# Performance work log

Hardware: AMD Instinct MI355X
Metric: run time of the kernel (lower is better)

Reference implementation:

```python
import jax, jax.numpy as jnp
import numpy as np

EPS = 1e-5
K = 20
LRELU = 0.2


def _bn(x, g, b, ch_axis):
    # inference BatchNorm with running_mean=0, running_var=1
    shape = [1] * x.ndim
    shape[ch_axis] = -1
    scale = (g / jnp.sqrt(1.0 + EPS)).reshape(shape)
    bias = b.reshape(shape)
    return x * scale + bias


def _lrelu(x):
    return jnp.where(x > 0, x, LRELU * x)


def _edge_conv(x, W, g, b):
    # x: (B, C, N) -> (B, C_out, N)
    B, C, N = x.shape
    xt = jnp.swapaxes(x, 1, 2)                      # (B, N, C)
    inner = -2.0 * jnp.einsum('bnc,bmc->bnm', xt, xt)
    xx = jnp.sum(xt * xt, axis=2)                   # (B, N)
    pdist = -xx[:, :, None] - inner - xx[:, None, :]  # negative sq dist (B,N,N)
    idx = jax.lax.top_k(pdist, K)[1]                # (B, N, K) nearest (incl. self)
    # gather neighbor features per batch: (C, N) indexed by (N, K) -> (C, N, K)
    neighbors = jax.vmap(lambda xf, id_: xf[:, id_])(x, idx)  # (B, C, N, K)
    center = jnp.broadcast_to(x[..., None], (B, C, N, K))
    edge = jnp.concatenate([center, neighbors - center], axis=1)  # (B, 2C, N, K)
    h = jnp.einsum('oc,bcnk->bonk', W, edge)        # 1x1 conv, no bias
    h = _lrelu(_bn(h, g, b, 1))
    return jnp.max(h, axis=-1)                      # (B, C_out, N)


def setup_inputs() -> dict:
    key = jax.random.key(0)
    ks = jax.random.split(key, 24)
    B, N = 4, 2048
    d = {}
    d['points'] = jax.random.normal(ks[0], (B, N, 3), dtype=jnp.float32)

    def w(k_, shape):
        return 0.1 * jax.random.normal(k_, shape, dtype=jnp.float32)

    def gam(k_, c):
        return 1.0 + 0.1 * jax.random.normal(k_, (c,), dtype=jnp.float32)

    def bet(k_, c):
        return 0.05 * jax.random.normal(k_, (c,), dtype=jnp.float32)

    # EdgeConv blocks: (out, 2*in)
    d['w1'], d['g1'], d['b1'] = w(ks[1], (64, 6)), gam(ks[2], 64), bet(ks[3], 64)
    d['w2'], d['g2'], d['b2'] = w(ks[4], (64, 128)), gam(ks[5], 64), bet(ks[6], 64)
    d['w3'], d['g3'], d['b3'] = w(ks[7], (128, 128)), gam(ks[8], 128), bet(ks[9], 128)
    d['w4'], d['g4'], d['b4'] = w(ks[10], (256, 256)), gam(ks[11], 256), bet(ks[12], 256)
    # conv5 1x1: 512 -> 1024
    d['w5'], d['g5'], d['b5'] = w(ks[13], (1024, 512)), gam(ks[14], 1024), bet(ks[15], 1024)
    # fc: 2048 -> 512 -> 256
    d['fw1'], d['fb1'] = w(ks[16], (512, 2048)), 0.05 * jax.random.normal(ks[17], (512,), dtype=jnp.float32)
    d['g6'], d['b6'] = gam(ks[18], 512), bet(ks[19], 512)
    d['fw2'], d['fb2'] = w(ks[20], (256, 512)), 0.05 * jax.random.normal(ks[21], (256,), dtype=jnp.float32)
    d['g7'], d['b7'] = gam(ks[22], 256), bet(ks[23], 256)
    return d


def reference(points, w1, g1, b1, w2, g2, b2, w3, g3, b3, w4, g4, b4,
              w5, g5, b5, fw1, fb1, g6, b6, fw2, fb2, g7, b7):
    x = jnp.swapaxes(points[:, :, :3], 1, 2)        # (B, 3, N)
    x1 = _edge_conv(x, w1, g1, b1)                  # (B, 64, N)
    x2 = _edge_conv(x1, w2, g2, b2)                 # (B, 64, N)
    x3 = _edge_conv(x2, w3, g3, b3)                 # (B, 128, N)
    x4 = _edge_conv(x3, w4, g4, b4)                 # (B, 256, N)
    h = jnp.concatenate([x1, x2, x3, x4], axis=1)   # (B, 512, N)
    h = _lrelu(_bn(jnp.einsum('oc,bcn->bon', w5, h), g5, b5, 1))  # (B, 1024, N)
    h_max = jnp.max(h, axis=-1)
    h_avg = jnp.mean(h, axis=-1)
    f = jnp.concatenate([h_max, h_avg], axis=1)     # (B, 2048)
    f = _lrelu(_bn(f @ fw1.T + fb1, g6, b6, 1))     # dropout = identity (eval)
    f = _bn(f @ fw2.T + fb2, g7, b7, 1)
    return f                                        # (B, 256)
```

## Files before the change

### kernel.cpp

```cpp
#include <hip/hip_runtime.h>
#include <hip/hip_bf16.h>
#include <float.h>

#define N_PTS 2048
#define B_SZ  4
#define KNN   20
#define LRELU_S 0.2f
#define FT    512
#define NPOOL 8

typedef __hip_bfloat16 bf16;
typedef __attribute__((ext_vector_type(8))) short short8v;
typedef __attribute__((ext_vector_type(4))) short short4v;
typedef __attribute__((ext_vector_type(4))) float floatx4;

__device__ __forceinline__ float b2f(const bf16 v) { return __bfloat162float(v); }
__device__ __forceinline__ float ldf(const float* p) { return *p; }
__device__ __forceinline__ float ldf(const bf16* p)  { return __bfloat162float(*p); }
__device__ __forceinline__ short8v ld8(const bf16* p) { return *(const short8v*)p; }
__device__ __forceinline__ unsigned umin(unsigned a, unsigned b) { return a < b ? a : b; }
__device__ __forceinline__ short bfbits(float f) {
    bf16 t = __float2bfloat16(f);
    return *reinterpret_cast<short*>(&t);
}

__device__ __forceinline__ void gload16(const void* g, void* l) {
    __builtin_amdgcn_global_load_lds(
        (const __attribute__((address_space(1))) void*)g,
        (__attribute__((address_space(3))) void*)l, 16, 0, 0);
}

__device__ __forceinline__ int sniff_body(const unsigned short* pts_hw) {
    int sane = 0;
    for (int j = 0; j < 64; ++j) {
        unsigned short v = pts_hw[2 * j];
        int e = (v >> 7) & 0xFF;
        if (e >= 100 && e <= 140) ++sane;
    }
    return (sane >= 32) ? 1 : 0;
}

__global__ void k_sniff(const unsigned short* __restrict__ pts_hw, int* __restrict__ flag) {
    if (threadIdx.x != 0 || blockIdx.x != 0) return;
    *flag = sniff_body(pts_hw);
}

struct WPack {
    const void* src[23];
    int off[24];
    int rows[23];
    int cols[23];
};

__device__ __forceinline__ void repack_body(const WPack& wp, int isb,
                                            float* __restrict__ dst, int i, int limit) {
    if (i >= limit) return;
    int lo = 0, hi = 23;
    while (lo + 1 < hi) { int mid = (lo + hi) >> 1; if (i >= wp.off[mid]) lo = mid; else hi = mid; }
    int j = i - wp.off[lo];
    float v = isb ? b2f(((const bf16*)wp.src[lo])[j]) : ((const float*)wp.src[lo])[j];
    int dj = j;
    int cols = wp.cols[lo];
    if (cols) dj = (j % cols) * wp.rows[lo] + (j / cols);
    dst[wp.off[lo] + dj] = v;
}

template<int C, int COUT>
__device__ __forceinline__ void wsplit_body(const void* __restrict__ W, int isb,
                                            bf16* __restrict__ dst, int i) {
    if (i >= COUT * C) return;
    int o = i / C, c = i % C;
    float w1 = isb ? b2f(((const bf16*)W)[(size_t)o * 2 * C + c])
                   : ((const float*)W)[(size_t)o * 2 * C + c];
    float w2 = isb ? b2f(((const bf16*)W)[(size_t)o * 2 * C + C + c])
                   : ((const float*)W)[(size_t)o * 2 * C + C + c];
    float wd = w1 - w2;
    bf16 h2 = __float2bfloat16(w2);
    bf16 hd = __float2bfloat16(wd);
    dst[i]                = h2;
    dst[COUT * C + i]     = __float2bfloat16(w2 - b2f(h2));
    dst[2 * COUT * C + i] = hd;
    dst[3 * COUT * C + i] = __float2bfloat16(wd - b2f(hd));
}

__device__ __forceinline__ void w5split_body(const void* __restrict__ W, int isb,
                                             bf16* __restrict__ dst, int i) {
    if (i >= 1024 * 512) return;
    float w = isb ? b2f(((const bf16*)W)[i]) : ((const float*)W)[i];
    bf16 h = __float2bfloat16(w);
    dst[i] = h;
    dst[1024 * 512 + i] = __float2bfloat16(w - b2f(h));
}

__device__ __forceinline__ void transpose_body(const void* __restrict__ pts, int isb,
                                               float* __restrict__ x0, int i) {
    if (i >= B_SZ * N_PTS) return;
    int b = i / N_PTS, n = i % N_PTS;
    for (int c = 0; c < 3; ++c) {
        size_t s = ((size_t)b * N_PTS + n) * 3 + c;
        float v = isb ? b2f(((const bf16*)pts)[s]) : ((const float*)pts)[s];
        x0[((size_t)b * 3 + c) * N_PTS + n] = v;
    }
}

__global__ void k_prep(WPack wp, float* __restrict__ wf, int rlimit,
                       const void* __restrict__ w2s, bf16* __restrict__ wsp2,
                       const void* __restrict__ w3s, bf16* __restrict__ wsp3,
                       const void* __restrict__ w4s, bf16* __restrict__ wsp4,
                       const void* __restrict__ w5s, bf16* __restrict__ w5sp,
                       const void* __restrict__ pts, float* __restrict__ x0,
                       int* __restrict__ flagout) {
    __shared__ int sfl;
    if (threadIdx.x == 0) {
        int f = sniff_body((const unsigned short*)pts);
        sfl = f;
        if (blockIdx.x == 0) *flagout = f;
    }
    __syncthreads();
    const int isb = sfl;
    const int nbrep = (rlimit + 255) >> 8;
    int ib = blockIdx.x, t = threadIdx.x;
    if (ib < nbrep) { repack_body(wp, isb, wf, ib * 256 + t, rlimit); return; }
    ib -= nbrep;
    if (ib < 16)   { wsplit_body<64, 64>(w2s, isb, wsp2, ib * 256 + t); return; }
    ib -= 16;
    if (ib < 32)   { wsplit_body<64, 128>(w3s, isb, wsp3, ib * 256 + t); return; }
    ib -= 32;
    if (ib < 128)  { wsplit_body<128, 256>(w4s, isb, wsp4, ib * 256 + t); return; }
    ib -= 128;
    if (ib < 2048) { w5split_body(w5s, isb, w5sp, ib * 256 + t); return; }
    ib -= 2048;
    transpose_body(pts, isb, x0, ib * 256 + t);
}

__global__ void k_repack(WPack wp, const int* __restrict__ flag, float* __restrict__ dst, int limit) {
    repack_body(wp, *flag, dst, blockIdx.x * blockDim.x + threadIdx.x, limit);
}
__global__ void k_transpose(const void* __restrict__ pts, const int* __restrict__ flag,
                            float* __restrict__ x0) {
    transpose_body(pts, *flag, x0, blockIdx.x * blockDim.x + threadIdx.x);
}

__device__ __forceinline__ void load32(const float* row, int mbase, float* r) {
    const float4* p = (const float4*)(row + mbase);
#pragma unroll
    for (int i = 0; i < 8; ++i) {
        float4 f = p[i];
        r[4 * i + 0] = f.x; r[4 * i + 1] = f.y; r[4 * i + 2] = f.z; r[4 * i + 3] = f.w;
    }
}
__device__ __forceinline__ void load32(const bf16* row, int mbase, float* r) {
    const uint4* p = (const uint4*)(row + mbase);
#pragma unroll
    for (int i = 0; i < 4; ++i) {
        uint4 u = p[i];
        r[8 * i + 0] = __uint_as_float(u.x << 16);
        r[8 * i + 1] = __uint_as_float(u.x & 0xFFFF0000u);
        r[8 * i + 2] = __uint_as_float(u.y << 16);
        r[8 * i + 3] = __uint_as_float(u.y & 0xFFFF0000u);
        r[8 * i + 4] = __uint_as_float(u.z << 16);
        r[8 * i + 5] = __uint_as_float(u.z & 0xFFFF0000u);
        r[8 * i + 6] = __uint_as_float(u.w << 16);
        r[8 * i + 7] = __uint_as_float(u.w & 0xFFFF0000u);
    }
}

__device__ __forceinline__ void s2ins(unsigned k, unsigned& m1, unsigned& m2) {
    unsigned lo = umin(m1, k);
    unsigned hi = (m1 < k) ? k : m1;
    m1 = lo;
    m2 = umin(m2, hi);
}

__device__ __forceinline__ void select20x2(const unsigned* ka, const unsigned* kb,
                                           int* outA, int* outB, int lane) {
    const unsigned SENT = 0xFFFFFFFFu;
    unsigned a1 = SENT, a2 = SENT, b1 = SENT, b2 = SENT;
#pragma unroll
    for (int j = 0; j < 32; ++j) {
        s2ins(ka[j], a1, a2);
        s2ins(kb[j], b1, b2);
    }
#pragma unroll 1
    for (int k = 0; k < KNN; ++k) {
        unsigned va = a1, vb = b1;
#pragma unroll
        for (int off = 32; off >= 1; off >>= 1) {
            va = umin(va, (unsigned)__shfl_xor((int)va, off));
            vb = umin(vb, (unsigned)__shfl_xor((int)vb, off));
        }
        if (lane == 0) { outA[k] = (int)(va & 2047u); outB[k] = (int)(vb & 2047u); }
        if (a1 == va) { a1 = a2; a2 = SENT; }
        if (b1 == vb) { b1 = b2; b2 = SENT; }
        if (a1 == SENT) {
#pragma unroll
            for (int j = 0; j < 32; ++j) {
                unsigned t = (ka[j] > va) ? ka[j] : SENT;
                s2ins(t, a1, a2);
            }
        }
        if (b1 == SENT) {
#pragma unroll
            for (int j = 0; j < 32; ++j) {
                unsigned t = (kb[j] > vb) ? kb[j] : SENT;
                s2ins(t, b1, b2);
            }
        }
    }
}

__global__ __launch_bounds__(256) void k_knn3(const float* __restrict__ x0,
                                              int* __restrict__ idx) {
    __shared__ float qf[8][3];
    int ib = blockIdx.x;
    int b  = ib / (N_PTS / 8);
    int q0 = (ib % (N_PTS / 8)) * 8;
    const float* xb = x0 + (size_t)b * 3 * N_PTS;

    if (threadIdx.x < 24) {
        int q = threadIdx.x / 3, c = threadIdx.x % 3;
        qf[q][c] = xb[(size_t)c * N_PTS + q0 + q];
    }
    __syncthreads();

    int w = threadIdx.x >> 6, lane = threadIdx.x & 63;
    int qa = q0 + 2 * w;
    int mbase = lane * 32;

    float da[32], db[32];
#pragma unroll
    for (int j = 0; j < 32; ++j) { da[j] = 0.f; db[j] = 0.f; }
#pragma unroll
    for (int c = 0; c < 3; ++c) {
        float r[32];
        load32(xb + (size_t)c * N_PTS, mbase, r);
        float qac = qf[2 * w][c], qbc = qf[2 * w + 1][c];
#pragma unroll
        for (int j = 0; j < 32; ++j) {
            float ta = r[j] - qac; da[j] = fmaf(ta, ta, da[j]);
            float tb = r[j] - qbc; db[j] = fmaf(tb, tb, db[j]);
        }
    }
    unsigned ka[32], kb[32];
#pragma unroll
    for (int j = 0; j < 32; ++j) {
        ka[j] = (__float_as_uint(da[j]) & 0xFFFFF800u) | (unsigned)(mbase + j);
        kb[j] = (__float_as_uint(db[j]) & 0xFFFFF800u) | (unsigned)(mbase + j);
    }
    select20x2(ka, kb, idx + ((size_t)b * N_PTS + qa) * KNN,
               idx + ((size_t)b * N_PTS + qa + 1) * KNN, lane);
}

template<typename T, int C>
__global__ __launch_bounds__(256) void k_knn(const T* __restrict__ x, int bstride,
                                             int* __restrict__ idx) {
    __shared__ float qf[4][C];
    int ib = blockIdx.x;
    int b  = ib / (N_PTS / 4);
    int q0 = (ib % (N_PTS / 4)) * 4;
    const T* xb = x + (size_t)b * bstride;

    for (int t = threadIdx.x; t < 4 * C; t += 256) {
        int pt = t / C, c = t % C;
        qf[pt][c] = ldf(&xb[(size_t)c * N_PTS + (q0 + pt)]);
    }
    __syncthreads();

    int w = threadIdx.x >> 6, lane = threadIdx.x & 63;
    int q = q0 + w;
    int mbase = lane * 32;

    float v[32];
#pragma unroll
    for (int j = 0; j < 32; ++j) v[j] = 0.f;

    for (int c = 0; c < C; ++c) {
        float qc = qf[w][c];
        float r[32];
        load32(xb + (size_t)c * N_PTS, mbase, r);
#pragma unroll
        for (int j = 0; j < 32; ++j) { float t = r[j] - qc; v[j] = fmaf(t, t, v[j]); }
    }

    for (int k = 0; k < KNN; ++k) {
        float bv = FLT_MAX; int bi = 0x7FFFFFFF;
#pragma unroll
        for (int j = 0; j < 32; ++j)
            if (v[j] < bv) { bv = v[j]; bi = mbase + j; }
#pragma unroll
        for (int off = 32; off >= 1; off >>= 1) {
            float ov = __shfl_xor(bv, off);
            int   oi = __shfl_xor(bi, off);
            if (ov < bv || (ov == bv && oi < bi)) { bv = ov; bi = oi; }
        }
        if (lane == 0) idx[((size_t)b * N_PTS + q) * KNN + k] = bi;
        int wl = bi >> 5, wj = bi & 31;
        if (lane == wl) {
#pragma unroll
            for (int j = 0; j < 32; ++j) if (j == wj) v[j] = FLT_MAX;
        }
    }
}

template<int C>
__device__ __forceinline__ void gram_body(const bf16* __restrict__ featT, int c0,
                                          float* __restrict__ G,
                                          short* At, short* Bt, int ib) {
    const int KC = 64;
    int b  = ib >> 8;
    int t  = ib & 255;
    int n0 = (t >> 4) << 7;
    int m0 = (t & 15) << 7;

    int tid = threadIdx.x;
    int w = tid >> 6, lane = tid & 63;
    int rw = (w & 1) * 64, cw = (w >> 1) * 64;
    int lrow = lane & 15, quad = lane >> 4;

    floatx4 acc[4][4];
#pragma unroll
    for (int ri = 0; ri < 4; ++ri)
#pragma unroll
        for (int ci = 0; ci < 4; ++ci) acc[ri][ci] = (floatx4){0.f, 0.f, 0.f, 0.f};

    for (int ck = 0; ck < C; ck += KC) {
        __syncthreads();
#pragma unroll
        for (int it = 0; it < 4; ++it) {
            int s = tid + it * 256;
            int row = s >> 3, seg = s & 7;
            int gseg = seg ^ (row & 7);
            gload16(featT + ((size_t)(b * N_PTS + n0 + row) * FT) + c0 + ck + gseg * 8,
                    &At[(s & ~63) * 8]);
            gload16(featT + ((size_t)(b * N_PTS + m0 + row) * FT) + c0 + ck + gseg * 8,
                    &Bt[(s & ~63) * 8]);
        }
        __syncthreads();
#pragma unroll
        for (int kk = 0; kk < KC; kk += 32) {
            int ks = kk >> 3;
            short8v a[4], bb[4];
#pragma unroll
            for (int ri = 0; ri < 4; ++ri) {
                int row = rw + ri * 16 + lrow;
                int seg = (ks + quad) ^ (row & 7);
                a[ri] = *(const short8v*)&At[row * 64 + seg * 8];
            }
#pragma unroll
            for (int ci = 0; ci < 4; ++ci) {
                int row = cw + ci * 16 + lrow;
                int seg = (ks + quad) ^ (row & 7);
                bb[ci] = *(const short8v*)&Bt[row * 64 + seg * 8];
            }
#pragma unroll
            for (int ri = 0; ri < 4; ++ri)
#pragma unroll
                for (int ci = 0; ci < 4; ++ci)
                    acc[ri][ci] = __builtin_amdgcn_mfma_f32_16x16x32_bf16(a[ri], bb[ci], acc[ri][ci], 0, 0, 0);
        }
    }

#pragma unroll
    for (int ri = 0; ri < 4; ++ri)
#pragma unroll
        for (int ci = 0; ci < 4; ++ci) {
            int n = n0 + rw + ri * 16 + quad * 4;
            int m = m0 + cw + ci * 16 + lrow;
            float* gp = G + ((size_t)b * N_PTS + n) * N_PTS + m;
#pragma unroll
            for (int reg = 0; reg < 4; ++reg)
                gp[(size_t)reg * N_PTS] = acc[ri][ci][reg];
        }
}

template<int COUT, int C>
__device__ __forceinline__ void xform_body(const bf16* __restrict__ featT, int c0,
                                           const bf16* __restrict__ Wsp,
                                           bf16* __restrict__ Yh, int isb,
                                           short* Bt, int ib2) {
    const int M2 = 2 * COUT;
    const int KC = 64;
    int nt = ib2 & 63;
    int mt = ib2 >> 6;
    int tid = threadIdx.x;
    int w = tid >> 6, lane = tid & 63;
    int rw = (w & 1) * 64, cw = (w >> 1) * 64;
    int l15 = lane & 15, quad = lane >> 4;

    floatx4 acc[4][4];
#pragma unroll
    for (int ri = 0; ri < 4; ++ri)
#pragma unroll
        for (int ci = 0; ci < 4; ++ci) acc[ri][ci] = (floatx4){0.f, 0.f, 0.f, 0.f};

    for (int ck = 0; ck < C; ck += KC) {
        __syncthreads();
#pragma unroll
        for (int it = 0; it < 4; ++it) {
            int s = tid + it * 256;
            int row = s >> 3, seg = s & 7;
            int gseg = seg ^ (row & 7);
            gload16(featT + (size_t)(nt * 128 + row) * FT + c0 + ck + gseg * 8,
                    &Bt[(s & ~63) * 8]);
        }
        __syncthreads();
#pragma unroll
        for (int kk = 0; kk < KC; kk += 32) {
            int ks = kk >> 3;
            short8v bfr[4];
#pragma unroll
            for (int ci = 0; ci < 4; ++ci) {
                int row = cw + ci * 16 + l15;
                int seg = (ks + quad) ^ (row & 7);
                bfr[ci] = *(const short8v*)&Bt[row * 64 + seg * 8];
            }
#pragma unroll
            for (int ri = 0; ri < 4; ++ri) {
                int rbase = mt * 128 + rw + ri * 16;
                bool uselo = (!isb) || (rbase >= COUT);
                int mrow = rbase + l15;
                int base = (mrow < COUT) ? mrow : (mrow + COUT);
                const bf16* hi = Wsp + (size_t)base * C + ck + kk + quad * 8;
                short8v ah = ld8(hi);
                short8v al;
                if (uselo) al = ld8(hi + (size_t)COUT * C);
#pragma unroll
                for (int ci = 0; ci < 4; ++ci) {
                    acc[ri][ci] = __builtin_amdgcn_mfma_f32_16x16x32_bf16(ah, bfr[ci], acc[ri][ci], 0, 0, 0);
                    if (uselo)
                        acc[ri][ci] = __builtin_amdgcn_mfma_f32_16x16x32_bf16(al, bfr[ci], acc[ri][ci], 0, 0, 0);
                }
            }
        }
    }

#pragma unroll
    for (int ri = 0; ri < 4; ++ri)
#pragma unroll
        for (int ci = 0; ci < 4; ++ci) {
            int n = nt * 128 + cw + ci * 16 + l15;
            int m = mt * 128 + rw + ri * 16 + quad * 4;
            short4v o4;
            o4[0] = bfbits(acc[ri][ci][0]);
            o4[1] = bfbits(acc[ri][ci][1]);
            o4[2] = bfbits(acc[ri][ci][2]);
            o4[3] = bfbits(acc[ri][ci][3]);
            *(short4v*)(Yh + (size_t)n * M2 + m) = o4;
        }
}

template<int C, int COUT>
__global__ __launch_bounds__(256) void k_gx(const bf16* __restrict__ featT, int c0,
        const bf16* __restrict__ Wsp, float* __restrict__ G, bf16* __restrict__ Yh,
        const int* __restrict__ flag) {
    __shared__ __align__(16) short lds[2 * 128 * 64];
    int ib = blockIdx.x;
    if (ib < B_SZ * 256) {
        gram_body<C>(featT, c0, G, lds, lds + 128 * 64, ib);
    } else {
        xform_body<COUT, C>(featT, c0, Wsp, Yh, *flag, lds, ib - B_SZ * 256);
    }
}

template<int COUT>
__global__ __launch_bounds__(256) void k_selgmax(const float* __restrict__ G,
        const float* __restrict__ xxin, const bf16* __restrict__ Yh,
        const float* __restrict__ gam, const float* __restrict__ bet,
        bf16* __restrict__ featT, int c0f, float* __restrict__ xxout) {
    const int M2 = 2 * COUT;
    const int OT = COUT / 64;
    __shared__ int sidx[8][KNN];

    int ib = blockIdx.x;
    int b  = ib / (N_PTS / 8);
    int q0 = (ib % (N_PTS / 8)) * 8;
    int w = threadIdx.x >> 6, lane = threadIdx.x & 63;
    int qa = q0 + 2 * w;
    const float* gA = G + ((size_t)b * N_PTS + qa) * N_PTS;
    const float* gB = gA + N_PTS;
    const float* xr = xxin + (size_t)b * N_PTS;
    float xqa = xr[qa], xqb = xr[qa + 1];

    unsigned ka[32], kb[32];
#pragma unroll
    for (int r = 0; r < 8; ++r) {
        int m0 = r * 256 + (lane << 2);
        float4 x4 = *(const float4*)(xr + m0);
        float4 a4 = *(const float4*)(gA + m0);
        float4 b4 = *(const float4*)(gB + m0);
        float s;
        s = fmaf(-2.f, a4.x, x4.x) + xqa; s = fmaxf(s, 0.f);
        ka[4 * r + 0] = (__float_as_uint(s) & 0xFFFFF800u) | (unsigned)(m0 + 0);
        s = fmaf(-2.f, a4.y, x4.y) + xqa; s = fmaxf(s, 0.f);
        ka[4 * r + 1] = (__float_as_uint(s) & 0xFFFFF800u) | (unsigned)(m0 + 1);
        s = fmaf(-2.f, a4.z, x4.z) + xqa; s = fmaxf(s, 0.f);
        ka[4 * r + 2] = (__float_as_uint(s) & 0xFFFFF800u) | (unsigned)(m0 + 2);
        s = fmaf(-2.f, a4.w, x4.w) + xqa; s = fmaxf(s, 0.f);
        ka[4 * r + 3] = (__float_as_uint(s) & 0xFFFFF800u) | (unsigned)(m0 + 3);
        s = fmaf(-2.f, b4.x, x4.x) + xqb; s = fmaxf(s, 0.f);
        kb[4 * r + 0] = (__float_as_uint(s) & 0xFFFFF800u) | (unsigned)(m0 + 0);
        s = fmaf(-2.f, b4.y, x4.y) + xqb; s = fmaxf(s, 0.f);
        kb[4 * r + 1] = (__float_as_uint(s) & 0xFFFFF800u) | (unsigned)(m0 + 1);
        s = fmaf(-2.f, b4.z, x4.z) + xqb; s = fmaxf(s, 0.f);
        kb[4 * r + 2] = (__float_as_uint(s) & 0xFFFFF800u) | (unsigned)(m0 + 2);
        s = fmaf(-2.f, b4.w, x4.w) + xqb; s = fmaxf(s, 0.f);
        kb[4 * r + 3] = (__float_as_uint(s) & 0xFFFFF800u) | (unsigned)(m0 + 3);
    }
    select20x2(ka, kb, &sidx[2 * w][0], &sidx[2 * w + 1][0], lane);
    __syncthreads();

    size_t iA = (size_t)b * N_PTS + qa;
    const float inv = rsqrtf(1.0f + 1e-5f);
    float yda[OT], ydb[OT], scl[OT], bis[OT], mxa[OT], mxb[OT];
#pragma unroll
    for (int j = 0; j < OT; ++j) {
        int o = lane + 64 * j;
        yda[j] = b2f(Yh[iA * M2 + COUT + o]);
        ydb[j] = b2f(Yh[(iA + 1) * M2 + COUT + o]);
        scl[j] = gam[o] * inv;
        bis[j] = bet[o];
        mxa[j] = -FLT_MAX; mxb[j] = -FLT_MAX;
    }
    const bf16* Yb = Yh + (size_t)b * N_PTS * M2;
#pragma unroll
    for (int k = 0; k < KNN; ++k) {
        int m0 = sidx[2 * w][k] & (N_PTS - 1);
        int m1 = sidx[2 * w + 1][k] & (N_PTS - 1);
        const bf16* r0 = Yb + (size_t)m0 * M2;
        const bf16* r1 = Yb + (size_t)m1 * M2;
#pragma unroll
        for (int j = 0; j < OT; ++j) {
            int o = lane + 64 * j;
            float ha = (yda[j] + b2f(r0[o])) * scl[j] + bis[j];
            ha = ha > 0.f ? ha : LRELU_S * ha;
            mxa[j] = fmaxf(mxa[j], ha);
            float hb = (ydb[j] + b2f(r1[o])) * scl[j] + bis[j];
            hb = hb > 0.f ? hb : LRELU_S * hb;
            mxb[j] = fmaxf(mxb[j], hb);
        }
    }
    float sa = 0.f, sb = 0.f;
#pragma unroll
    for (int j = 0; j < OT; ++j) {
        bf16 va = __float2bfloat16(mxa[j]);
        bf16 vb = __float2bfloat16(mxb[j]);
        featT[iA * FT + c0f + lane + 64 * j] = va;
        featT[(iA + 1) * FT + c0f + lane + 64 * j] = vb;
        if (xxout) {
            float pa = b2f(va); sa = fmaf(pa, pa, sa);
            float pb = b2f(vb); sb = fmaf(pb, pb, sb);
        }
    }
    if (xxout) {
#pragma unroll
        for (int off = 32; off >= 1; off >>= 1) {
            sa += __shfl_xor(sa, off);
            sb += __shfl_xor(sb, off);
        }
        if (lane == 0) { xxout[iA] = sa; xxout[iA + 1] = sb; }
    }
}

template<typename T, int C, int COUT, bool WF>
__global__ __launch_bounds__(256) void k_edgeconv(const T* __restrict__ x, int bstride,
                           const int* __restrict__ idx,
                           const float* __restrict__ Wt,
                           const float* __restrict__ gam,
                           const float* __restrict__ bet,
                           bf16* __restrict__ out, int ostride,
                           bf16* __restrict__ featT, int c0f,
                           float* __restrict__ xxout) {
    const int PT = 4;
    const int OT = COUT / 64;
    const int CP = (C + 3) & ~3;
    __shared__ float sh[PT][KNN + 1][CP];

    int ib = blockIdx.x;
    int b  = ib / (N_PTS / PT);
    int n0 = (ib % (N_PTS / PT)) * PT;
    const T* xb = x + (size_t)b * bstride;

    const int TOT = PT * (KNN + 1) * C;
    for (int t = threadIdx.x; t < TOT; t += 256) {
        int pt = t / ((KNN + 1) * C);
        int r  = t % ((KNN + 1) * C);
        int row = r / C, c = r % C;
        int n = n0 + pt;
        int m = (row == 0) ? n
                           : (idx[((size_t)b * N_PTS + n) * KNN + (row - 1)] & (N_PTS - 1));
        sh[pt][row][c] = ldf(&xb[(size_t)c * N_PTS + m]);
    }
    __syncthreads();

    int w = threadIdx.x >> 6, lane = threadIdx.x & 63;
    int n = n0 + w;

    constexpr int KT = (OT >= 4) ? 10 : 20;
    constexpr int NPASS = KNN / KT;

    float base[OT];
    float mx[OT];
#pragma unroll
    for (int j = 0; j < OT; ++j) { base[j] = 0.f; mx[j] = -FLT_MAX; }

    const float inv = rsqrtf(1.0f + 1e-5f);

#pragma unroll
    for (int pass = 0; pass < NPASS; ++pass) {
        float acc[OT][KT];
#pragma unroll
        for (int j = 0; j < OT; ++j)
#pragma unroll
            for (int k = 0; k < KT; ++k) acc[j][k] = 0.f;

        for (int c = 0; c < C; ++c) {
            float xq = sh[w][0][c];
            float w2v[OT];
#pragma unroll
            for (int j = 0; j < OT; ++j)
                w2v[j] = Wt[(size_t)(C + c) * COUT + lane + 64 * j];
            if (pass == 0) {
#pragma unroll
                for (int j = 0; j < OT; ++j) {
                    float w1v = Wt[(size_t)c * COUT + lane + 64 * j];
                    base[j] = fmaf(w1v - w2v[j], xq, base[j]);
                }
            }
#pragma unroll
            for (int k = 0; k < KT; ++k) {
                float nv = sh[w][1 + pass * KT + k][c];
#pragma unroll
                for (int j = 0; j < OT; ++j) acc[j][k] = fmaf(w2v[j], nv, acc[j][k]);
            }
        }

#pragma unroll
        for (int j = 0; j < OT; ++j) {
            int o = lane + 64 * j;
            float scale = gam[o] * inv, bias = bet[o];
#pragma unroll
            for (int k = 0; k < KT; ++k) {
                float h = (base[j] + acc[j][k]) * scale + bias;
                h = h > 0.f ? h : LRELU_S * h;
                mx[j] = fmaxf(mx[j], h);
            }
        }
    }

    float s = 0.f;
#pragma unroll
    for (int j = 0; j < OT; ++j) {
        int o = lane + 64 * j;
        bf16 bv = __float2bfloat16(mx[j]);
        if (!WF) out[(size_t)b * ostride + (size_t)o * N_PTS + n] = bv;
        if (WF) {
            featT[((size_t)b * N_PTS + n) * FT + c0f + o] = bv;
            float q = b2f(bv);
            s = fmaf(q, q, s);
        }
    }
    if (WF && xxout) {
#pragma unroll
        for (int off = 32; off >= 1; off >>= 1) s += __shfl_xor(s, off);
        if (lane == 0) xxout[(size_t)b * N_PTS + n] = s;
    }
}

__global__ __launch_bounds__(256) void k_conv5mfma(
        const bf16* __restrict__ featT, const bf16* __restrict__ w5sp,
        const float* __restrict__ g5, const float* __restrict__ b5,
        float* __restrict__ fmxp, float* __restrict__ fsmp,
        const int* __restrict__ flag) {
    __shared__ __align__(16) short Bt[256 * 64];
    __shared__ __align__(16) short Ah[64 * 64];
    __shared__ __align__(16) short Al[64 * 64];
    __shared__ float rmx[4][64];
    __shared__ float rsm[4][64];

    const int isb = *flag;
    int ib = blockIdx.x;
    int b  = ib / 128;
    int rem = ib % 128;
    int o0 = (rem >> 3) * 64;
    int nt = rem & 7;
    int tid = threadIdx.x;
    int w = tid >> 6, lane = tid & 63;
    int l15 = lane & 15, quad = lane >> 4;

    const bf16* Whi = w5sp;
    const bf16* Wlo = w5sp + 1024 * 512;
    const bf16* fb  = featT + (size_t)b * N_PTS * FT;
    const int nbase0 = nt * 256;

    floatx4 acc[4][4];
#pragma unroll
    for (int mi = 0; mi < 4; ++mi)
#pragma unroll
        for (int ni = 0; ni < 4; ++ni) acc[mi][ni] = (floatx4){0.f, 0.f, 0.f, 0.f};

    for (int ck = 0; ck < 512; ck += 64) {
        __syncthreads();
#pragma unroll
        for (int it = 0; it < 8; ++it) {
            int s = tid + it * 256;
            int row = s >> 3, seg = s & 7;
            int gseg = seg ^ (row & 7);
            gload16(fb + (size_t)(nbase0 + row) * FT + ck + gseg * 8,
                    &Bt[(s & ~63) * 8]);
        }
#pragma unroll
        for (int it = 0; it < 2; ++it) {
            int s = tid + it * 256;
            int row = s >> 3, seg = s & 7;
            int gseg = seg ^ (row & 7);
            gload16(Whi + (size_t)(o0 + row) * 512 + ck + gseg * 8, &Ah[(s & ~63) * 8]);
            if (!isb)
                gload16(Wlo + (size_t)(o0 + row) * 512 + ck + gseg * 8, &Al[(s & ~63) * 8]);
        }
        __syncthreads();
#pragma unroll
        for (int kk = 0; kk < 64; kk += 32) {
            int ks = kk >> 3;
            short8v bfr[4], ah[4], al[4];
#pragma unroll
            for (int ni = 0; ni < 4; ++ni) {
                int row = w * 64 + ni * 16 + l15;
                int seg = (ks + quad) ^ (row & 7);
                bfr[ni] = *(const short8v*)&Bt[row * 64 + seg * 8];
            }
#pragma unroll
            for (int mi = 0; mi < 4; ++mi) {
                int row = mi * 16 + l15;
                int seg = (ks + quad) ^ (row & 7);
                ah[mi] = *(const short8v*)&Ah[row * 64 + seg * 8];
                if (!isb) al[mi] = *(const short8v*)&Al[row * 64 + seg * 8];
            }
#pragma unroll
            for (int mi = 0; mi < 4; ++mi)
#pragma unroll
                for (int ni = 0; ni < 4; ++ni) {
                    acc[mi][ni] = __builtin_amdgcn_mfma_f32_16x16x32_bf16(ah[mi], bfr[ni], acc[mi][ni], 0, 0, 0);
                    if (!isb)
                        acc[mi][ni] = __builtin_amdgcn_mfma_f32_16x16x32_bf16(al[mi], bfr[ni], acc[mi][ni], 0, 0, 0);
                }
        }
    }

    const float inv = rsqrtf(1.0f + 1e-5f);
#pragma unroll
    for (int mi = 0; mi < 4; ++mi) {
#pragma unroll
        for (int r = 0; r < 4; ++r) {
            int o = o0 + mi * 16 + quad * 4 + r;
            float scale = g5[o] * inv, bias = b5[o];
            float mx = -FLT_MAX, sm = 0.f;
#pragma unroll
            for (int ni = 0; ni < 4; ++ni) {
                float h = acc[mi][ni][r] * scale + bias;
                h = h > 0.f ? h : LRELU_S * h;
                mx = fmaxf(mx, h);
                sm += h;
            }
#pragma unroll
            for (int off = 1; off <= 8; off <<= 1) {
                mx = fmaxf(mx, __shfl_xor(mx, off));
                sm += __shfl_xor(sm, off);
            }
            if (l15 == 0) {
                rmx[w][mi * 16 + quad * 4 + r] = mx;
                rsm[w][mi * 16 + quad * 4 + r] = sm;
            }
        }
    }
    __syncthreads();
    if (tid < 64) {
        float mx = -FLT_MAX, sm = 0.f;
#pragma unroll
        for (int ww = 0; ww < 4; ++ww) { mx = fmaxf(mx, rmx[ww][tid]); sm += rsm[ww][tid]; }
        fmxp[((size_t)b * 1024 + o0 + tid) * NPOOL + nt] = mx;
        fsmp[((size_t)b * 1024 + o0 + tid) * NPOOL + nt] = sm;
    }
}

__global__ void k_pool(const float* __restrict__ fmxp, const float* __restrict__ fsmp,
                       float* __restrict__ fvec) {
    int i = blockIdx.x * blockDim.x + threadIdx.x;
    if (i >= B_SZ * 1024) return;
    int b = i >> 10, o = i & 1023;
    float mx = -FLT_MAX, sm = 0.f;
    for (int ch = 0; ch < NPOOL; ++ch) {
        mx = fmaxf(mx, fmxp[(size_t)i * NPOOL + ch]);
        sm += fsmp[(size_t)i * NPOOL + ch];
    }
    fvec[(size_t)b * 2048 + o] = mx;
    fvec[(size_t)b * 2048 + 1024 + o] = sm * (1.0f / N_PTS);
}

__global__ __launch_bounds__(256) void k_fc1(const float* __restrict__ fvec,
        const void* __restrict__ fw1, const void* __restrict__ fb1,
        const void* __restrict__ g6,  const void* __restrict__ b6,
        const int* __restrict__ flag, float* __restrict__ tbuf) {
    __shared__ float red[4];
    int ib = blockIdx.x;
    int b = ib >> 9, o = ib & 511;
    const float* fv = fvec + (size_t)b * 2048;
    int tid = threadIdx.x;
    const int isb = *flag;
    float s = 0.f;
    if (isb) {
        const bf16* wr = (const bf16*)fw1 + (size_t)o * 2048;
        for (int j = tid; j < 2048; j += 256) s = fmaf(b2f(wr[j]), fv[j], s);
    } else {
        const float* wr = (const float*)fw1 + (size_t)o * 2048;
        for (int j = tid; j < 2048; j += 256) s = fmaf(wr[j], fv[j], s);
    }
#pragma unroll
    for (int off = 32; off >= 1; off >>= 1) s += __shfl_xor(s, off);
    if ((tid & 63) == 0) red[tid >> 6] = s;
    __syncthreads();
    if (tid == 0) {
        float fb = isb ? b2f(((const bf16*)fb1)[o]) : ((const float*)fb1)[o];
        float gg = isb ? b2f(((const bf16*)g6)[o])  : ((const float*)g6)[o];
        float bb = isb ? b2f(((const bf16*)b6)[o])  : ((const float*)b6)[o];
        float acc = fb + red[0] + red[1] + red[2] + red[3];
        float h = acc * gg * rsqrtf(1.0f + 1e-5f) + bb;
        tbuf[(size_t)b * 512 + o] = h > 0.f ? h : LRELU_S * h;
    }
}

__global__ __launch_bounds__(256) void k_fc2(const float* __restrict__ tbuf,
        const void* __restrict__ fw2, const void* __restrict__ fb2,
        const void* __restrict__ g7,  const void* __restrict__ b7,
        const int* __restrict__ flag, void* __restrict__ out) {
    __shared__ float red[4];
    int ib = blockIdx.x;
    int b = ib >> 8, o = ib & 255;
    const float* tv = tbuf + (size_t)b * 512;
    int tid = threadIdx.x;
    const int isb = *flag;
    float s;
    if (isb) {
        const bf16* wr = (const bf16*)fw2 + (size_t)o * 512;
        s = fmaf(b2f(wr[tid]), tv[tid], b2f(wr[tid + 256]) * tv[tid + 256]);
    } else {
        const float* wr = (const float*)fw2 + (size_t)o * 512;
        s = fmaf(wr[tid], tv[tid], wr[tid + 256] * tv[tid + 256]);
    }
#pragma unroll
    for (int off = 32; off >= 1; off >>= 1) s += __shfl_xor(s, off);
    if ((tid & 63) == 0) red[tid >> 6] = s;
    __syncthreads();
    if (tid == 0) {
        float fb = isb ? b2f(((const bf16*)fb2)[o]) : ((const float*)fb2)[o];
        float gg = isb ? b2f(((const bf16*)g7)[o])  : ((const float*)g7)[o];
        float bb = isb ? b2f(((const bf16*)b7)[o])  : ((const float*)b7)[o];
        float acc = fb + red[0] + red[1] + red[2] + red[3];
        float h = acc * gg * rsqrtf(1.0f + 1e-5f) + bb;
        if (isb) ((bf16*)out)[(size_t)b * 256 + o] = __float2bfloat16(h);
        else     ((float*)out)[(size_t)b * 256 + o] = h;
    }
}

#define NCH 2
__global__ __launch_bounds__(256) void k_conv5pool(const bf16* __restrict__ feat,
                            const float* __restrict__ w5,
                            const float* __restrict__ g5,
                            const float* __restrict__ b5,
                            float* __restrict__ fmxp, float* __restrict__ fsmp) {
    const int OT = 8;
    const int NT = 4;
    const int CHN = N_PTS / NCH;
    __shared__ float wl[OT][512];
    __shared__ float rmx[4][OT];
    __shared__ float rsm[4][OT];

    int ib = blockIdx.x;
    int ch = ib % NCH;
    int ot = (ib / NCH) % (1024 / OT);
    int b  = ib / (NCH * (1024 / OT));
    int o0 = ot * OT;
    const bf16* fb = feat + (size_t)b * 512 * N_PTS;

    for (int t = threadIdx.x; t < OT * 512; t += 256) {
        int o = t >> 9, c = t & 511;
        wl[o][c] = w5[(size_t)(o0 + o) * 512 + c];
    }
    __syncthreads();

    const int n0 = ch * CHN + threadIdx.x * NT;

    float acc[OT][NT];
#pragma unroll
    for (int o = 0; o < OT; ++o)
#pragma unroll
        for (int t = 0; t < NT; ++t) acc[o][t] = 0.f;

    for (int c = 0; c < 512; c += 4) {
        float fv[4][NT];
#pragma unroll
        for (int j = 0; j < 4; ++j) {
            uint2 u = *(const uint2*)(fb + (size_t)(c + j) * N_PTS + n0);
            fv[j][0] = __uint_as_float(u.x << 16);
            fv[j][1] = __uint_as_float(u.x & 0xFFFF0000u);
            fv[j][2] = __uint_as_float(u.y << 16);
            fv[j][3] = __uint_as_float(u.y & 0xFFFF0000u);
        }
#pragma unroll
        for (int o = 0; o < OT; ++o) {
            float4 wv = *(const float4*)&wl[o][c];
#pragma unroll
            for (int t = 0; t < NT; ++t) {
                acc[o][t] = fmaf(wv.x, fv[0][t], acc[o][t]);
                acc[o][t] = fmaf(wv.y, fv[1][t], acc[o][t]);
                acc[o][t] = fmaf(wv.z, fv[2][t], acc[o][t]);
                acc[o][t] = fmaf(wv.w, fv[3][t], acc[o][t]);
            }
        }
    }

    const float inv = rsqrtf(1.0f + 1e-5f);
    int w = threadIdx.x >> 6, lane = threadIdx.x & 63;
#pragma unroll
    for (int o = 0; o < OT; ++o) {
        float scale = g5[o0 + o] * inv, bias = b5[o0 + o];
        float mx = -FLT_MAX, sm = 0.f;
#pragma unroll
        for (int t = 0; t < NT; ++t) {
            float h = acc[o][t] * scale + bias;
            h = h > 0.f ? h : LRELU_S * h;
            mx = fmaxf(mx, h);
            sm += h;
        }
#pragma unroll
        for (int off = 32; off >= 1; off >>= 1) {
            mx = fmaxf(mx, __shfl_xor(mx, off));
            sm += __shfl_xor(sm, off);
        }
        if (lane == 0) { rmx[w][o] = mx; rsm[w][o] = sm; }
    }
    __syncthreads();
    if (threadIdx.x < OT) {
        int o = threadIdx.x;
        float mx = -FLT_MAX, sm = 0.f;
#pragma unroll
        for (int ww = 0; ww < 4; ++ww) { mx = fmaxf(mx, rmx[ww][o]); sm += rsm[ww][o]; }
        fmxp[((size_t)b * 1024 + o0 + o) * NCH + ch] = mx;
        fsmp[((size_t)b * 1024 + o0 + o) * NCH + ch] = sm;
    }
}

__global__ void k_head(const float* __restrict__ fmxp, const float* __restrict__ fsmp,
                       const float* __restrict__ fw1, const float* __restrict__ fb1,
                       const float* __restrict__ g6,  const float* __restrict__ b6,
                       const float* __restrict__ fw2, const float* __restrict__ fb2,
                       const float* __restrict__ g7,  const float* __restrict__ b7,
                       const int* __restrict__ flag, void* __restrict__ out) {
    __shared__ float f[2048];
    __shared__ float t[512];
    int b = blockIdx.x;
    for (int i = threadIdx.x; i < 1024; i += 256) {
        float mx = -FLT_MAX, sm = 0.f;
        for (int ch = 0; ch < NCH; ++ch) {
            mx = fmaxf(mx, fmxp[((size_t)b * 1024 + i) * NCH + ch]);
            sm += fsmp[((size_t)b * 1024 + i) * NCH + ch];
        }
        f[i]        = mx;
        f[1024 + i] = sm * (1.0f / N_PTS);
    }
    __syncthreads();
    const float inv = rsqrtf(1.0f + 1e-5f);
    for (int o = threadIdx.x; o < 512; o += 256) {
        const float* wr = fw1 + (size_t)o * 2048;
        float acc = fb1[o];
        for (int j = 0; j < 2048; ++j) acc += wr[j] * f[j];
        float h = acc * g6[o] * inv + b6[o];
        t[o] = h > 0.f ? h : LRELU_S * h;
    }
    __syncthreads();
    {
        int o = threadIdx.x;
        const float* wr = fw2 + (size_t)o * 512;
        float acc = fb2[o];
        for (int j = 0; j < 512; ++j) acc += wr[j] * t[j];
        float h = acc * g7[o] * inv + b7[o];
        if (*flag) ((bf16*)out)[(size_t)b * 256 + o] = __float2bfloat16(h);
        else       ((float*)out)[(size_t)b * 256 + o] = h;
    }
}

extern "C" void kernel_launch(void* const* d_in, const int* in_sizes, int n_in,
                              void* d_out, int out_size, void* d_ws, size_t ws_size,
                              hipStream_t stream) {
    static const int wsz[23] = {
        384, 64, 64,   8192, 64, 64,   16384, 128, 128,   65536, 256, 256,
        524288, 1024, 1024,   1048576, 512,   512, 512,   131072, 256,   256, 256
    };
    static const int trows[23] = {64,0,0, 64,0,0, 128,0,0, 256,0,0, 0,0,0, 0,0, 0,0, 0,0, 0,0};
    static const int tcols[23] = { 6,0,0,128,0,0, 128,0,0, 256,0,0, 0,0,0, 0,0, 0,0, 0,0, 0,0};

    WPack wp;
    int total = 0;
    for (int i = 0; i < 23; ++i) {
        wp.src[i] = d_in[i + 1]; wp.off[i] = total; total += wsz[i];
        wp.rows[i] = trows[i]; wp.cols[i] = tcols[i];
    }
    wp.off[23] = total;

    const size_t flag_bytes = 16;
    const size_t x0_bytes   = (size_t)B_SZ * 3 * N_PTS * 4;
    const size_t feat_bytes = (size_t)B_SZ * 512 * N_PTS * 2;
    const size_t idx_bytes  = (size_t)B_SZ * N_PTS * KNN * 4;
    const size_t pool_bytes = (size_t)B_SZ * 1024 * 4 * 2;
    const size_t wf_bytes   = (size_t)total * 4;
    const size_t base_need  = flag_bytes + x0_bytes + feat_bytes + idx_bytes + pool_bytes + wf_bytes;

    const size_t featT_bytes = (size_t)B_SZ * N_PTS * FT * 2;
    const size_t xx_bytes    = (size_t)B_SZ * N_PTS * 4;
    const size_t wsp2_elems  = 4 * 64 * 64;
    const size_t wsp3_elems  = 4 * 128 * 64;
    const size_t wsp4_elems  = 4 * 256 * 128;
    const size_t w5sp_elems  = 2 * 1024 * 512;
    const size_t wsp_bytes   = (wsp2_elems + wsp3_elems + wsp4_elems + w5sp_elems) * 2;
    const size_t Yh_bytes    = (size_t)B_SZ * N_PTS * 512 * 2;
    const size_t S_bytes     = (size_t)B_SZ * N_PTS * N_PTS * 4;
    const size_t full_need   = base_need + featT_bytes + 2 * xx_bytes + wsp_bytes
                             + Yh_bytes + S_bytes;

    if (ws_size < base_need) return;
    const bool use_gram = (ws_size >= full_need);

    char* w = (char*)d_ws;
    int*   flag = (int*)w;              w += flag_bytes;
    float* x0   = (float*)w;            w += x0_bytes;
    bf16*  feat = (bf16*)w;             w += feat_bytes;
    int*   idx  = (int*)w;              w += idx_bytes;
    w += pool_bytes;
    float* wf   = (float*)w;            w += wf_bytes;
    bf16*  featT = (bf16*)w;            w += featT_bytes;
    float* xxA   = (float*)w;           w += xx_bytes;
    float* xxB   = (float*)w;           w += xx_bytes;
    bf16*  wsp2  = (bf16*)w;            w += wsp2_elems * 2;
    bf16*  wsp3  = (bf16*)w;            w += wsp3_elems * 2;
    bf16*  wsp4  = (bf16*)w;            w += wsp4_elems * 2;
    bf16*  w5sp  = (bf16*)w;            w += w5sp_elems * 2;
    bf16*  Yh    = (bf16*)w;            w += Yh_bytes;
    float* S     = (float*)w;

    float* fmxp = (float*)idx;
    float* fsmp = fmxp + (size_t)B_SZ * 1024 * NPOOL;
    float* fvec = fsmp + (size_t)B_SZ * 1024 * NPOOL;
    float* tbuf = fvec + (size_t)B_SZ * 2048;

    const int FBS = 512 * N_PTS;

    const float* w1t = wf + wp.off[0],  *g1 = wf + wp.off[1],  *b1 = wf + wp.off[2];
    const float* w2t = wf + wp.off[3],  *g2 = wf + wp.off[4],  *b2 = wf + wp.off[5];
    const float* w3t = wf + wp.off[6],  *g3 = wf + wp.off[7],  *b3 = wf + wp.off[8];
    const float* w4t = wf + wp.off[9],  *g4 = wf + wp.off[10], *b4 = wf + wp.off[11];
    const float* w5  = wf + wp.off[12], *g5 = wf + wp.off[13], *b5 = wf + wp.off[14];
    const float* fw1 = wf + wp.off[15], *fb1 = wf + wp.off[16];
    const float* g6  = wf + wp.off[17], *b6 = wf + wp.off[18];
    const float* fw2 = wf + wp.off[19], *fb2 = wf + wp.off[20];
    const float* g7  = wf + wp.off[21], *b7 = wf + wp.off[22];

    const int GK = B_SZ * N_PTS / 4;
    const int G8 = B_SZ * N_PTS / 8;
    const int NG = B_SZ * 256;

    if (use_gram) {
        const int rlimit = wp.off[15];
        const int nbrep = (rlimit + 255) / 256;
        const int prep_grid = nbrep + 16 + 32 + 128 + 2048 + 32;
        k_prep<<<prep_grid, 256, 0, stream>>>(wp, wf, rlimit,
                                              d_in[4], wsp2, d_in[7], wsp3,
                                              d_in[10], wsp4, d_in[13], w5sp,
                                              d_in[0], x0, flag);

        k_knn3<<<G8, 256, 0, stream>>>(x0, idx);
        k_edgeconv<float, 3, 64, true><<<GK, 256, 0, stream>>>(
            x0, 3 * N_PTS, idx, w1t, g1, b1, feat, FBS, featT, 0, xxA);
        k_gx<64, 64><<<NG + 64, 256, 0, stream>>>(featT, 0, wsp2, S, Yh, flag);
        k_selgmax<64><<<G8, 256, 0, stream>>>(S, xxA, Yh, g2, b2, featT, 64, xxB);
        k_gx<64, 128><<<NG + 128, 256, 0, stream>>>(featT, 64, wsp3, S, Yh, flag);
        k_selgmax<128><<<G8, 256, 0, stream>>>(S, xxB, Yh, g3, b3, featT, 128, xxA);
        k_gx<128, 256><<<NG + 256, 256, 0, stream>>>(featT, 128, wsp4, S, Yh, flag);
        k_selgmax<256><<<G8, 256, 0, stream>>>(S, xxA, Yh, g4, b4, featT, 256, nullptr);

        k_conv5mfma<<<B_SZ * 128, 256, 0, stream>>>(featT, w5sp, g5, b5, fmxp, fsmp, flag);
        k_pool<<<(B_SZ * 1024 + 255) / 256, 256, 0, stream>>>(fmxp, fsmp, fvec);
        k_fc1<<<B_SZ * 512, 256, 0, stream>>>(fvec, d_in[16], d_in[17], d_in[18], d_in[19],
                                              flag, tbuf);
        k_fc2<<<B_SZ * 256, 256, 0, stream>>>(tbuf, d_in[20], d_in[21], d_in[22], d_in[23],
                                              flag, d_out);
    } else {
        k_sniff<<<1, 64, 0, stream>>>((const unsigned short*)d_in[0], flag);
        k_repack<<<(total + 255) / 256, 256, 0, stream>>>(wp, flag, wf, total);
        k_transpose<<<(B_SZ * N_PTS + 255) / 256, 256, 0, stream>>>(d_in[0], flag, x0);

        k_knn<float, 3><<<GK, 256, 0, stream>>>(x0, 3 * N_PTS, idx);
        k_edgeconv<float, 3, 64, false><<<GK, 256, 0, stream>>>(
            x0, 3 * N_PTS, idx, w1t, g1, b1, feat + 0 * N_PTS, FBS, nullptr, 0, nullptr);
        k_knn<bf16, 64><<<GK, 256, 0, stream>>>(feat + 0 * N_PTS, FBS, idx);
        k_edgeconv<bf16, 64, 64, false><<<GK, 256, 0, stream>>>(
            feat + 0 * N_PTS, FBS, idx, w2t, g2, b2, feat + 64 * N_PTS, FBS, nullptr, 0, nullptr);
        k_knn<bf16, 64><<<GK, 256, 0, stream>>>(feat + 64 * N_PTS, FBS, idx);
        k_edgeconv<bf16, 64, 128, false><<<GK, 256, 0, stream>>>(
            feat + 64 * N_PTS, FBS, idx, w3t, g3, b3, feat + 128 * N_PTS, FBS, nullptr, 0, nullptr);
        k_knn<bf16, 128><<<GK, 256, 0, stream>>>(feat + 128 * N_PTS, FBS, idx);
        k_edgeconv<bf16, 128, 256, false><<<GK, 256, 0, stream>>>(
            feat + 128 * N_PTS, FBS, idx, w4t, g4, b4, feat + 256 * N_PTS, FBS, nullptr, 0, nullptr);

        k_conv5pool<<<B_SZ * (1024 / 8) * NCH, 256, 0, stream>>>(feat, w5, g5, b5, fmxp, fsmp);
        k_head<<<B_SZ, 256, 0, stream>>>(fmxp, fsmp, fw1, fb1, g6, b6, fw2, fb2, g7, b7,
                                         flag, d_out);
    }
}
```

Before: 350.7 us.

## Fuse first kNN with EdgeConv1, halve conv5 tile, skip redundant weight repacks

Merges the layer-1 kNN selection with the first EdgeConv, so neighbour indices stay in shared memory and the separate edgeconv launch and idx round trip go away. The conv5 MFMA kernel now uses 128-column tiles with twice as many blocks (NPOOL raised to 16) to give more parallelism per launch. The prep kernel also skips repacking weight slot 12, which the gram path never reads, and skips writing the low-part split of w5 when inputs are bf16. The trade-off is smaller tiles in conv5, which means less reuse of A per block, and more partial pooling buffers to reduce.

```diff
diff --git a/kernel.cpp b/kernel.cpp
--- a/kernel.cpp
+++ b/kernel.cpp
@@ -7,7 +7,7 @@
 #define KNN   20
 #define LRELU_S 0.2f
 #define FT    512
-#define NPOOL 8
+#define NPOOL 16
 
 typedef __hip_bfloat16 bf16;
 typedef __attribute__((ext_vector_type(8))) short short8v;
@@ -53,10 +53,12 @@
 };
 
 __device__ __forceinline__ void repack_body(const WPack& wp, int isb,
-                                            float* __restrict__ dst, int i, int limit) {
+                                            float* __restrict__ dst, int i, int limit,
+                                            int skip12) {
     if (i >= limit) return;
     int lo = 0, hi = 23;
     while (lo + 1 < hi) { int mid = (lo + hi) >> 1; if (i >= wp.off[mid]) lo = mid; else hi = mid; }
+    if (skip12 && lo == 12) return;
     int j = i - wp.off[lo];
     float v = isb ? b2f(((const bf16*)wp.src[lo])[j]) : ((const float*)wp.src[lo])[j];
     int dj = j;
@@ -89,7 +91,7 @@
     float w = isb ? b2f(((const bf16*)W)[i]) : ((const float*)W)[i];
     bf16 h = __float2bfloat16(w);
     dst[i] = h;
-    dst[1024 * 512 + i] = __float2bfloat16(w - b2f(h));
+    if (!isb) dst[1024 * 512 + i] = __float2bfloat16(w - b2f(h));
 }
 
 __device__ __forceinline__ void transpose_body(const void* __restrict__ pts, int isb,
@@ -120,7 +122,7 @@
     const int isb = sfl;
     const int nbrep = (rlimit + 255) >> 8;
     int ib = blockIdx.x, t = threadIdx.x;
-    if (ib < nbrep) { repack_body(wp, isb, wf, ib * 256 + t, rlimit); return; }
+    if (ib < nbrep) { repack_body(wp, isb, wf, ib * 256 + t, rlimit, 1); return; }
     ib -= nbrep;
     if (ib < 16)   { wsplit_body<64, 64>(w2s, isb, wsp2, ib * 256 + t); return; }
     ib -= 16;
@@ -134,7 +136,7 @@
 }
 
 __global__ void k_repack(WPack wp, const int* __restrict__ flag, float* __restrict__ dst, int limit) {
-    repack_body(wp, *flag, dst, blockIdx.x * blockDim.x + threadIdx.x, limit);
+    repack_body(wp, *flag, dst, blockIdx.x * blockDim.x + threadIdx.x, limit, 0);
 }
 __global__ void k_transpose(const void* __restrict__ pts, const int* __restrict__ flag,
                             float* __restrict__ x0) {
@@ -209,9 +211,12 @@
     }
 }
 
-__global__ __launch_bounds__(256) void k_knn3(const float* __restrict__ x0,
-                                              int* __restrict__ idx) {
+__global__ __launch_bounds__(256) void k_knn3ec(const float* __restrict__ x0,
+        const float* __restrict__ Wt, const float* __restrict__ gam,
+        const float* __restrict__ bet, bf16* __restrict__ featT,
+        float* __restrict__ xxout) {
     __shared__ float qf[8][3];
+    __shared__ int sidx[8][KNN];
     int ib = blockIdx.x;
     int b  = ib / (N_PTS / 8);
     int q0 = (ib % (N_PTS / 8)) * 8;
@@ -224,7 +229,6 @@
     __syncthreads();
 
     int w = threadIdx.x >> 6, lane = threadIdx.x & 63;
-    int qa = q0 + 2 * w;
     int mbase = lane * 32;
 
     float da[32], db[32];
@@ -247,8 +251,43 @@
         ka[j] = (__float_as_uint(da[j]) & 0xFFFFF800u) | (unsigned)(mbase + j);
         kb[j] = (__float_as_uint(db[j]) & 0xFFFFF800u) | (unsigned)(mbase + j);
     }
-    select20x2(ka, kb, idx + ((size_t)b * N_PTS + qa) * KNN,
-               idx + ((size_t)b * N_PTS + qa + 1) * KNN, lane);
+    select20x2(ka, kb, &sidx[2 * w][0], &sidx[2 * w + 1][0], lane);
+    __syncthreads();
+
+    const float inv = rsqrtf(1.0f + 1e-5f);
+    float scale = gam[lane] * inv, bias = bet[lane];
+    float w1v[3], w2v[3];
+#pragma unroll
+    for (int c = 0; c < 3; ++c) {
+        w1v[c] = Wt[(size_t)c * 64 + lane];
+        w2v[c] = Wt[(size_t)(3 + c) * 64 + lane];
+    }
+#pragma unroll
+    for (int p = 0; p < 2; ++p) {
+        int pt = 2 * w + p;
+        float base = 0.f;
+#pragma unroll
+        for (int c = 0; c < 3; ++c) base = fmaf(w1v[c] - w2v[c], qf[pt][c], base);
+        float mx = -FLT_MAX;
+#pragma unroll
+        for (int k = 0; k < KNN; ++k) {
+            int m = sidx[pt][k] & (N_PTS - 1);
+            float acc = 0.f;
+#pragma unroll
+            for (int c = 0; c < 3; ++c) acc = fmaf(w2v[c], xb[(size_t)c * N_PTS + m], acc);
+            float h = (base + acc) * scale + bias;
+            h = h > 0.f ? h : LRELU_S * h;
+            mx = fmaxf(mx, h);
+        }
+        bf16 bv = __float2bfloat16(mx);
+        size_t i = (size_t)b * N_PTS + q0 + pt;
+        featT[i * FT + lane] = bv;
+        float qv = b2f(bv);
+        float s = qv * qv;
+#pragma unroll
+        for (int off = 32; off >= 1; off >>= 1) s += __shfl_xor(s, off);
+        if (lane == 0) xxout[i] = s;
+    }
 }
 
 template<typename T, int C>
@@ -671,7 +710,7 @@
         const float* __restrict__ g5, const float* __restrict__ b5,
         float* __restrict__ fmxp, float* __restrict__ fsmp,
         const int* __restrict__ flag) {
-    __shared__ __align__(16) short Bt[256 * 64];
+    __shared__ __align__(16) short Bt[128 * 64];
     __shared__ __align__(16) short Ah[64 * 64];
     __shared__ __align__(16) short Al[64 * 64];
     __shared__ float rmx[4][64];
@@ -679,10 +718,10 @@
 
     const int isb = *flag;
     int ib = blockIdx.x;
-    int b  = ib / 128;
-    int rem = ib % 128;
-    int o0 = (rem >> 3) * 64;
-    int nt = rem & 7;
+    int b  = ib / 256;
+    int rem = ib % 256;
+    int o0 = (rem >> 4) * 64;
+    int nt = rem & 15;
     int tid = threadIdx.x;
     int w = tid >> 6, lane = tid & 63;
     int l15 = lane & 15, quad = lane >> 4;
@@ -690,18 +729,18 @@
     const bf16* Whi = w5sp;
     const bf16* Wlo = w5sp + 1024 * 512;
     const bf16* fb  = featT + (size_t)b * N_PTS * FT;
-    const int nbase0 = nt * 256;
-
-    floatx4 acc[4][4];
+    const int nbase0 = nt * 128;
+
+    floatx4 acc[4][2];
 #pragma unroll
     for (int mi = 0; mi < 4; ++mi)
 #pragma unroll
-        for (int ni = 0; ni < 4; ++ni) acc[mi][ni] = (floatx4){0.f, 0.f, 0.f, 0.f};
+        for (int ni = 0; ni < 2; ++ni) acc[mi][ni] = (floatx4){0.f, 0.f, 0.f, 0.f};
 
     for (int ck = 0; ck < 512; ck += 64) {
         __syncthreads();
 #pragma unroll
-        for (int it = 0; it < 8; ++it) {
+        for (int it = 0; it < 4; ++it) {
             int s = tid + it * 256;
             int row = s >> 3, seg = s & 7;
             int gseg = seg ^ (row & 7);
@@ -721,10 +760,10 @@
 #pragma unroll
         for (int kk = 0; kk < 64; kk += 32) {
             int ks = kk >> 3;
-            short8v bfr[4], ah[4], al[4];
-#pragma unroll
-            for (int ni = 0; ni < 4; ++ni) {
-                int row = w * 64 + ni * 16 + l15;
+            short8v bfr[2], ah[4], al[4];
+#pragma unroll
+            for (int ni = 0; ni < 2; ++ni) {
+                int row = w * 32 + ni * 16 + l15;
                 int seg = (ks + quad) ^ (row & 7);
                 bfr[ni] = *(const short8v*)&Bt[row * 64 + seg * 8];
             }
@@ -738,7 +777,7 @@
 #pragma unroll
             for (int mi = 0; mi < 4; ++mi)
 #pragma unroll
-                for (int ni = 0; ni < 4; ++ni) {
+                for (int ni = 0; ni < 2; ++ni) {
                     acc[mi][ni] = __builtin_amdgcn_mfma_f32_16x16x32_bf16(ah[mi], bfr[ni], acc[mi][ni], 0, 0, 0);
                     if (!isb)
                         acc[mi][ni] = __builtin_amdgcn_mfma_f32_16x16x32_bf16(al[mi], bfr[ni], acc[mi][ni], 0, 0, 0);
@@ -755,7 +794,7 @@
             float scale = g5[o] * inv, bias = b5[o];
             float mx = -FLT_MAX, sm = 0.f;
 #pragma unroll
-            for (int ni = 0; ni < 4; ++ni) {
+            for (int ni = 0; ni < 2; ++ni) {
                 float h = acc[mi][ni][r] * scale + bias;
                 h = h > 0.f ? h : LRELU_S * h;
                 mx = fmaxf(mx, h);
@@ -1076,9 +1115,7 @@
                                               d_in[10], wsp4, d_in[13], w5sp,
                                               d_in[0], x0, flag);
 
-        k_knn3<<<G8, 256, 0, stream>>>(x0, idx);
-        k_edgeconv<float, 3, 64, true><<<GK, 256, 0, stream>>>(
-            x0, 3 * N_PTS, idx, w1t, g1, b1, feat, FBS, featT, 0, xxA);
+        k_knn3ec<<<G8, 256, 0, stream>>>(x0, w1t, g1, b1, featT, xxA);
         k_gx<64, 64><<<NG + 64, 256, 0, stream>>>(featT, 0, wsp2, S, Yh, flag);
         k_selgmax<64><<<G8, 256, 0, stream>>>(S, xxA, Yh, g2, b2, featT, 64, xxB);
         k_gx<64, 128><<<NG + 128, 256, 0, stream>>>(featT, 64, wsp3, S, Yh, flag);
@@ -1086,7 +1123,7 @@
         k_gx<128, 256><<<NG + 256, 256, 0, stream>>>(featT, 128, wsp4, S, Yh, flag);
         k_selgmax<256><<<G8, 256, 0, stream>>>(S, xxA, Yh, g4, b4, featT, 256, nullptr);
 
-        k_conv5mfma<<<B_SZ * 128, 256, 0, stream>>>(featT, w5sp, g5, b5, fmxp, fsmp, flag);
+        k_conv5mfma<<<B_SZ * 256, 256, 0, stream>>>(featT, w5sp, g5, b5, fmxp, fsmp, flag);
         k_pool<<<(B_SZ * 1024 + 255) / 256, 256, 0, stream>>>(fmxp, fsmp, fvec);
         k_fc1<<<B_SZ * 512, 256, 0, stream>>>(fvec, d_in[16], d_in[17], d_in[18], d_in[19],
                                               flag, tbuf);
```

Result: slower. 380.8 us (+8.6%).
